# Performance work log

Measured on AMD Instinct MI355X. Metric: run time of the kernel, lower is better.

## Reference

```python
import jax, jax.numpy as jnp
import numpy as np

EPS = 1e-5

def _bilinear_sample(xb, ys, xs):
    # xb: [C,H,W]; ys, xs: [H,W] float sample coordinates (zero outside bounds)
    C, H, W = xb.shape
    y0 = jnp.floor(ys); x0 = jnp.floor(xs)
    y1 = y0 + 1.0;      x1 = x0 + 1.0
    wy1 = ys - y0; wy0 = 1.0 - wy1
    wx1 = xs - x0; wx0 = 1.0 - wx1
    def g(yi, xi):
        valid = (yi >= 0) & (yi < H) & (xi >= 0) & (xi < W)
        yc = jnp.clip(yi, 0, H - 1).astype(jnp.int32)
        xc = jnp.clip(xi, 0, W - 1).astype(jnp.int32)
        return xb[:, yc, xc] * valid[None].astype(xb.dtype)  # [C,H,W]
    return (g(y0, x0) * (wy0 * wx0)[None] + g(y0, x1) * (wy0 * wx1)[None]
          + g(y1, x0) * (wy1 * wx0)[None] + g(y1, x1) * (wy1 * wx1)[None])

def _deform_conv2d(x, offset, mask, w, b):
    # x:[B,C,H,W] offset:[B,18,H,W] mask:[B,9,H,W] w:[Co,C,3,3] b:[Co]
    B, C, H, W = x.shape
    Co = w.shape[0]
    ii = jnp.arange(H, dtype=x.dtype)[:, None]
    jj = jnp.arange(W, dtype=x.dtype)[None, :]
    cols = []
    for k in range(9):  # fixed 3x3 kernel positions, row-major (dy=offset[2k], dx=offset[2k+1])
        ky, kx = k // 3 - 1, k % 3 - 1
        ys = ii + ky + offset[:, 2 * k]      # [B,H,W]
        xs = jj + kx + offset[:, 2 * k + 1]
        v = jax.vmap(_bilinear_sample)(x, ys, xs)  # [B,C,H,W]
        cols.append(v * mask[:, k][:, None])
    cols = jnp.stack(cols, axis=1)               # [B,9,C,H,W]
    out = jnp.einsum('bkchw,ock->bohw', cols, w.reshape(Co, C, 9))
    return out + b[None, :, None, None]

def setup_inputs() -> dict:
    key = jax.random.key(0)
    k1, k2, k3, k4 = jax.random.split(key, 4)
    B, Cin, Cout, H, W = 8, 64, 64, 128, 128
    x = jax.random.normal(k1, (B, Cin, H, W), dtype=jnp.float32)
    # offset/mask conv: small weights so learned offsets stay O(1) pixels;
    # bias[18:]=2.0 as in the module's init (masks start near sigmoid(2))
    w_off = jax.random.normal(k2, (27, Cin, 3, 3), dtype=jnp.float32) * 0.01
    b_off = jnp.concatenate([jnp.zeros((18,), jnp.float32), jnp.full((9,), 2.0, jnp.float32)])
    w_dcn = jax.random.normal(k3, (Cout, Cin, 3, 3), dtype=jnp.float32) / np.sqrt(Cin * 9)
    b_dcn = jax.random.normal(k4, (Cout,), dtype=jnp.float32) * 0.01
    return {"x": x, "w_off": w_off, "b_off": b_off, "w_dcn": w_dcn, "b_dcn": b_dcn}

def reference(x, w_off, b_off, w_dcn, b_dcn):
    dn = ('NCHW', 'OIHW', 'NCHW')
    om = jax.lax.conv_general_dilated(x, w_off, (1, 1), 'SAME', dimension_numbers=dn)
    om = om + b_off[None, :, None, None]
    offset = om[:, :18]
    mask = jax.nn.sigmoid(om[:, 18:])
    y = _deform_conv2d(x, offset, mask, w_dcn, b_dcn)
    # InstanceNorm2d (affine=False, biased variance) + ReLU
    mu = jnp.mean(y, axis=(2, 3), keepdims=True)
    var = jnp.var(y, axis=(2, 3), keepdims=True)
    y = (y - mu) * jax.lax.rsqrt(var + EPS)
    return jax.nn.relu(y)
```

## Files before the change

kernel.cpp:

```cpp
#include <hip/hip_runtime.h>
#include <hip/hip_bf16.h>

#define BB   8
#define CIN  64
#define COUT 64
#define HH   128
#define WW   128
#define HWSZ (HH * WW)

typedef short bf16x8 __attribute__((ext_vector_type(8)));
typedef float f32x4  __attribute__((ext_vector_type(4)));
typedef float f32x2  __attribute__((ext_vector_type(2)));

__device__ __forceinline__ unsigned f2bf_u(float f) {
    unsigned u = __float_as_uint(f);
    return (u + 0x7fffu + ((u >> 16) & 1u)) >> 16;
}

__device__ __forceinline__ unsigned comb2(unsigned a, unsigned b, unsigned c, unsigned d,
                                          f32x2 W0, f32x2 W1, f32x2 W2, f32x2 W3) {
    f32x2 A = {__uint_as_float(a << 16), __uint_as_float(a & 0xffff0000u)};
    f32x2 B = {__uint_as_float(b << 16), __uint_as_float(b & 0xffff0000u)};
    f32x2 C = {__uint_as_float(c << 16), __uint_as_float(c & 0xffff0000u)};
    f32x2 D = {__uint_as_float(d << 16), __uint_as_float(d & 0xffff0000u)};
    f32x2 r = A * W0;
    r += B * W1;
    r += C * W2;
    r += D * W3;
    __hip_bfloat162 h = __float22bfloat162_rn(make_float2(r.x, r.y));
    return *(const unsigned*)&h;
}

__global__ __launch_bounds__(256) void k_tr(const float* __restrict__ x,
                                            const float* __restrict__ wd,
                                            const float* __restrict__ wof,
                                            unsigned short* __restrict__ xT,
                                            unsigned short* __restrict__ wdT,
                                            unsigned short* __restrict__ wofT)
{
    const int t = threadIdx.x;
    const int id = blockIdx.x;
    if (id >= 512) {
        int base = (id - 512) * 256 + t;
#pragma unroll
        for (int j = 0; j < 4; ++j) {
            int idx = base + j * 16384;
            if (idx < 36864) {
                int k = idx >> 12, rem = idx & 4095, co = rem >> 6, c = rem & 63;
                wdT[idx] = (unsigned short)f2bf_u(wd[(co * 64 + c) * 9 + k]);
            } else if (idx < 55296) {
                int jj = idx - 36864;
                int k = jj >> 11, rem = jj & 2047, o = rem >> 6, c = rem & 63;
                wofT[jj] = (o < 27) ? (unsigned short)f2bf_u(wof[(o * 64 + c) * 9 + k]) : 0;
            }
        }
        return;
    }
    __shared__ unsigned short tile[256 * 66];
    const int b = id & 7;
    const int p0 = (id >> 3) * 256;
#pragma unroll
    for (int i = 0; i < 16; ++i) {
        int c = i * 4 + (t >> 6);
        int pl = (t & 63) * 4;
        float4 v = *(const float4*)(x + (((size_t)b * 64 + c) << 14) + p0 + pl);
        tile[(pl + 0) * 66 + c] = (unsigned short)f2bf_u(v.x);
        tile[(pl + 1) * 66 + c] = (unsigned short)f2bf_u(v.y);
        tile[(pl + 2) * 66 + c] = (unsigned short)f2bf_u(v.z);
        tile[(pl + 3) * 66 + c] = (unsigned short)f2bf_u(v.w);
    }
    __syncthreads();
#pragma unroll
    for (int i = 0; i < 8; ++i) {
        int idd = i * 256 + t;
        int pt = idd >> 3, ck = idd & 7;
        const unsigned* srcp = (const unsigned*)&tile[pt * 66 + ck * 8];
        uint4 r;
        r.x = srcp[0]; r.y = srcp[1]; r.z = srcp[2]; r.w = srcp[3];
        *(uint4*)(xT + ((size_t)b << 20) + (size_t)(p0 + pt) * 64 + ck * 8) = r;
    }
}

__global__ __launch_bounds__(256, 2) void k_off(
    const unsigned short* __restrict__ xT, const unsigned short* __restrict__ wofT,
    const float* __restrict__ bof, float* __restrict__ om)
{
    __shared__ unsigned short tile[8 * 521 * 8];
    const int t = threadIdx.x;
    const int lane = t & 63, wv = t >> 6;
    const int q = lane >> 4, l15 = lane & 15;
    const int b = blockIdx.x & 7;
    const int xblk = blockIdx.x >> 3;
    const int h0 = xblk * 2;
    const int r0 = h0 - 1;
    const unsigned short* xb = xT + ((size_t)b << 20);

#pragma unroll
    for (int i = 0; i < 17; ++i) {
        int id = i * 256 + t;
        if (id < 4160) {
            int m = id & 7, lin = id >> 3;
            int row = lin / 130, col = lin % 130;
            int gy = r0 + row, gx = col - 1;
            uint4 v = {0u, 0u, 0u, 0u};
            if (((unsigned)gy < (unsigned)HH) && ((unsigned)gx < (unsigned)WW))
                v = *(const uint4*)(xb + ((size_t)(gy * WW + gx) << 6) + m * 8);
            *(uint4*)&tile[(m * 521 + lin) * 8] = v;
        }
    }
    __syncthreads();

    const int hrow = h0 + (wv >> 1);
    const int c0 = (wv & 1) * 64;

    f32x4 acc[2][4];
#pragma unroll
    for (int mt = 0; mt < 2; ++mt)
#pragma unroll
        for (int nt = 0; nt < 4; ++nt) acc[mt][nt] = (f32x4){0.f, 0.f, 0.f, 0.f};

#pragma unroll
    for (int k = 0; k < 9; ++k) {
        const int ky = k / 3 - 1, kx = k % 3 - 1;
        const int trow = (hrow - h0) + ky + 1;
        const unsigned short* wk = wofT + k * 2048;
#pragma unroll
        for (int ks = 0; ks < 2; ++ks) {
            bf16x8 af[2], bfr[4];
#pragma unroll
            for (int mt = 0; mt < 2; ++mt)
                af[mt] = *(const bf16x8*)(wk + (mt * 16 + l15) * 64 + ks * 32 + q * 8);
#pragma unroll
            for (int nt = 0; nt < 4; ++nt) {
                int tc = c0 + nt * 16 + l15 + kx + 1;
                bfr[nt] = *(const bf16x8*)&tile[((ks * 4 + q) * 521 + trow * 130 + tc) * 8];
            }
#pragma unroll
            for (int mt = 0; mt < 2; ++mt)
#pragma unroll
                for (int nt = 0; nt < 4; ++nt)
                    acc[mt][nt] = __builtin_amdgcn_mfma_f32_16x16x32_bf16(
                        af[mt], bfr[nt], acc[mt][nt], 0, 0, 0);
        }
    }

    const int p0 = xblk * 256 + wv * 64;
    float* omb = om + (size_t)b * 27 * HWSZ;
#pragma unroll
    for (int mt = 0; mt < 2; ++mt)
#pragma unroll
        for (int r = 0; r < 4; ++r) {
            int o = mt * 16 + q * 4 + r;
            if (o < 27) {
                float bias = bof[o];
#pragma unroll
                for (int nt = 0; nt < 4; ++nt) {
                    int pp = p0 + nt * 16 + l15;
                    float v = acc[mt][nt][r] + bias;
                    if (o >= 18) v = 1.f / (1.f + __expf(-v));
                    omb[(size_t)o * HWSZ + pp] = v;
                }
            }
        }
}

__global__ __launch_bounds__(256, 2) void k_dcn(
    const unsigned short* __restrict__ xT, const float* __restrict__ om,
    const unsigned short* __restrict__ wdT, const float* __restrict__ bd,
    float* __restrict__ out, float2* __restrict__ sums)
{
    __shared__ unsigned short col_sh[4][64 * 80];
    __shared__ unsigned       adr_sh[4][4][64];
    __shared__ float4         w_sh[4][64];
    __shared__ float          redS[4][64];
    __shared__ float          redQ[4][64];

    const int t = threadIdx.x;
    const int lane = t & 63, wv = t >> 6;
    const int q = lane >> 4, l15 = lane & 15;
    const int b = blockIdx.x & 7;
    const int pblk = (blockIdx.x >> 3) * 256;
    const int p = pblk + t;
    const int h = p >> 7, w = p & 127;
    const char* xbB = (const char*)(xT + ((size_t)b << 20));
    const float* omp = om + (size_t)b * 27 * HWSZ + p;
    const int gck = lane & 7;

    f32x4 acc[4][4];
#pragma unroll
    for (int mt = 0; mt < 4; ++mt)
#pragma unroll
        for (int nt = 0; nt < 4; ++nt) acc[mt][nt] = (f32x4){0.f, 0.f, 0.f, 0.f};

#define LOADG(P, g) { \
    int pt_ = (g) * 8 + (lane >> 3); \
    unsigned o0_ = adr_sh[wv][0][pt_]; \
    unsigned o1_ = adr_sh[wv][1][pt_]; \
    unsigned o2_ = adr_sh[wv][2][pt_]; \
    unsigned o3_ = adr_sh[wv][3][pt_]; \
    int bo_ = gck * 16; \
    P[0] = *(const uint4*)(xbB + o0_ + bo_); \
    P[1] = *(const uint4*)(xbB + o1_ + bo_); \
    P[2] = *(const uint4*)(xbB + o2_ + bo_); \
    P[3] = *(const uint4*)(xbB + o3_ + bo_); }

#define COMBG(P, g) { \
    int pt_ = (g) * 8 + (lane >> 3); \
    float4 w4_ = w_sh[wv][pt_]; \
    f32x2 W0_ = {w4_.x, w4_.x}, W1_ = {w4_.y, w4_.y}; \
    f32x2 W2_ = {w4_.z, w4_.z}, W3_ = {w4_.w, w4_.w}; \
    uint4 R_; \
    R_.x = comb2(P[0].x, P[1].x, P[2].x, P[3].x, W0_, W1_, W2_, W3_); \
    R_.y = comb2(P[0].y, P[1].y, P[2].y, P[3].y, W0_, W1_, W2_, W3_); \
    R_.z = comb2(P[0].z, P[1].z, P[2].z, P[3].z, W0_, W1_, W2_, W3_); \
    R_.w = comb2(P[0].w, P[1].w, P[2].w, P[3].w, W0_, W1_, W2_, W3_); \
    *(uint4*)&col_sh[wv][pt_ * 80 + gck * 8] = R_; }

    float offy = omp[0];
    float offx = omp[HWSZ];
    float mk   = omp[18 * HWSZ];

    for (int k = 0; k < 9; ++k) {
        float ys = (float)(h + (k / 3) - 1) + offy;
        float xs = (float)(w + (k % 3) - 1) + offx;
        float fy0 = floorf(ys), fx0 = floorf(xs);
        float wy1 = ys - fy0, wx1 = xs - fx0;
        float wy0 = 1.f - wy1, wx0 = 1.f - wx1;
        int y0 = (int)fy0, x0 = (int)fx0;
        int y1 = y0 + 1, x1 = x0 + 1;
        bool vy0 = (y0 >= 0) && (y0 < HH), vy1 = (y1 >= 0) && (y1 < HH);
        bool vx0 = (x0 >= 0) && (x0 < WW), vx1 = (x1 >= 0) && (x1 < WW);
        int y0c = min(max(y0, 0), HH - 1), y1c = min(max(y1, 0), HH - 1);
        int x0c = min(max(x0, 0), WW - 1), x1c = min(max(x1, 0), WW - 1);
        adr_sh[wv][0][lane] = (unsigned)((y0c * WW + x0c) << 7);
        adr_sh[wv][1][lane] = (unsigned)((y0c * WW + x1c) << 7);
        adr_sh[wv][2][lane] = (unsigned)((y1c * WW + x0c) << 7);
        adr_sh[wv][3][lane] = (unsigned)((y1c * WW + x1c) << 7);
        w_sh[wv][lane] = make_float4((vy0 && vx0) ? mk * wy0 * wx0 : 0.f,
                                     (vy0 && vx1) ? mk * wy0 * wx1 : 0.f,
                                     (vy1 && vx0) ? mk * wy1 * wx0 : 0.f,
                                     (vy1 && vx1) ? mk * wy1 * wx1 : 0.f);
        int kn = (k < 8) ? k + 1 : 8;
        offy = omp[(2 * kn) * HWSZ];
        offx = omp[(2 * kn + 1) * HWSZ];
        mk   = omp[(18 + kn) * HWSZ];
        __builtin_amdgcn_wave_barrier();

        const unsigned short* wk = wdT + k * 4096;
        bf16x8 af[2][4];
#pragma unroll
        for (int ks = 0; ks < 2; ++ks)
#pragma unroll
            for (int mt = 0; mt < 4; ++mt)
                af[ks][mt] = *(const bf16x8*)(wk + (mt * 16 + l15) * 64 + ks * 32 + q * 8);

        uint4 pb[3][4];
        LOADG(pb[0], 0);
        LOADG(pb[1], 1);
#pragma unroll
        for (int g = 0; g < 8; ++g) {
            if (g + 2 < 8) LOADG(pb[(g + 2) % 3], g + 2);
            COMBG(pb[g % 3], g);
        }
        __builtin_amdgcn_wave_barrier();

#pragma unroll
        for (int ks = 0; ks < 2; ++ks) {
            bf16x8 bfr[4];
#pragma unroll
            for (int nt = 0; nt < 4; ++nt)
                bfr[nt] = *(const bf16x8*)&col_sh[wv][(nt * 16 + l15) * 80 + ks * 32 + q * 8];
#pragma unroll
            for (int mt = 0; mt < 4; ++mt)
#pragma unroll
                for (int nt = 0; nt < 4; ++nt)
                    acc[mt][nt] = __builtin_amdgcn_mfma_f32_16x16x32_bf16(
                        af[ks][mt], bfr[nt], acc[mt][nt], 0, 0, 0);
        }
    }
#undef LOADG
#undef COMBG

    const int p0 = pblk + wv * 64;
    float* outb = out + (size_t)b * COUT * HWSZ;
#pragma unroll
    for (int mt = 0; mt < 4; ++mt)
#pragma unroll
        for (int r = 0; r < 4; ++r) {
            int co = mt * 16 + q * 4 + r;
            float bias = bd[co];
            float s = 0.f, qq = 0.f;
#pragma unroll
            for (int nt = 0; nt < 4; ++nt) {
                float v = acc[mt][nt][r] + bias;
                outb[(size_t)co * HWSZ + p0 + nt * 16 + l15] = v;
                s += v; qq += v * v;
            }
#pragma unroll
            for (int m = 1; m < 16; m <<= 1) {
                s += __shfl_xor(s, m);
                qq += __shfl_xor(qq, m);
            }
            if (l15 == 0) { redS[wv][co] = s; redQ[wv][co] = qq; }
        }
    __syncthreads();
    if (t < 64) {
        float S = redS[0][t] + redS[1][t] + redS[2][t] + redS[3][t];
        float Q = redQ[0][t] + redQ[1][t] + redQ[2][t] + redQ[3][t];
        atomicAdd(&sums[b * 64 + t].x, S);
        atomicAdd(&sums[b * 64 + t].y, Q);
    }
}

__global__ __launch_bounds__(256) void k_norm(float* __restrict__ out,
                                              const float2* __restrict__ sums)
{
    const int id = blockIdx.x;
    const int b = id & 7;
    const int rest = id >> 3;
    const int co = rest >> 4;
    const int off = rest & 15;
    const int bco = b * 64 + co;
    const int i = (bco << 12) + off * 256 + threadIdx.x;
    float2 sq = sums[bco];
    float mu  = sq.x * (1.f / (float)HWSZ);
    float var = sq.y * (1.f / (float)HWSZ) - mu * mu;
    float rstd = rsqrtf(var + 1e-5f);
    float4* o4 = (float4*)out;
    float4 v = o4[i];
    v.x = fmaxf((v.x - mu) * rstd, 0.f);
    v.y = fmaxf((v.y - mu) * rstd, 0.f);
    v.z = fmaxf((v.z - mu) * rstd, 0.f);
    v.w = fmaxf((v.w - mu) * rstd, 0.f);
    o4[i] = v;
}

extern "C" void kernel_launch(void* const* d_in, const int* in_sizes, int n_in,
                              void* d_out, int out_size, void* d_ws, size_t ws_size,
                              hipStream_t stream) {
    const float* x   = (const float*)d_in[0];
    const float* wof = (const float*)d_in[1];
    const float* bof = (const float*)d_in[2];
    const float* wd  = (const float*)d_in[3];
    const float* bd  = (const float*)d_in[4];
    float* out = (float*)d_out;

    char* ws = (char*)d_ws;
    unsigned short* xT   = (unsigned short*)ws;
    float*          om   = (float*)(ws + 16777216);
    unsigned short* wdT  = (unsigned short*)(ws + 30932992);
    unsigned short* wofT = (unsigned short*)(ws + 31006720);
    float2*         sums = (float2*)(ws + 31043584);

    hipMemsetAsync(sums, 0, 4096, stream);
    k_tr    <<<576, 256, 0, stream>>>(x, wd, wof, xT, wdT, wofT);
    k_off   <<<512, 256, 0, stream>>>(xT, wofT, bof, om);
    k_dcn   <<<512, 256, 0, stream>>>(xT, om, wdT, bd, out, sums);
    k_norm  <<<8192, 256, 0, stream>>>(out, (const float2*)sums);
}
```

Before: 173.6 us.

## Shuffle sample addresses via registers, shrink LDS, raise DCN occupancy, fold memset

Per-pixel bilinear addresses and weights are now passed between lanes with __shfl instead of being staged through per-wave LDS arrays. The column tile padding shrinks from 80 to 72 elements and launch bounds go from 2 to 4 blocks per CU. Together these cut LDS use and aim for more resident waves to hide gather latency. The sums buffer is now zeroed inside k_tr instead of by a separate hipMemsetAsync, removing one stream operation. Risks are register pressure at the higher occupancy target and more shuffle instructions in the inner loop.

```diff
diff --git a/kernel.cpp b/kernel.cpp
--- a/kernel.cpp
+++ b/kernel.cpp
@@ -36,11 +36,13 @@
                                             const float* __restrict__ wof,
                                             unsigned short* __restrict__ xT,
                                             unsigned short* __restrict__ wdT,
-                                            unsigned short* __restrict__ wofT)
+                                            unsigned short* __restrict__ wofT,
+                                            float4* __restrict__ sums4)
 {
     const int t = threadIdx.x;
     const int id = blockIdx.x;
     if (id >= 512) {
+        if (id == 512) sums4[t] = make_float4(0.f, 0.f, 0.f, 0.f);
         int base = (id - 512) * 256 + t;
 #pragma unroll
         for (int j = 0; j < 4; ++j) {
@@ -164,14 +166,12 @@
         }
 }
 
-__global__ __launch_bounds__(256, 2) void k_dcn(
+__global__ __launch_bounds__(256, 4) void k_dcn(
     const unsigned short* __restrict__ xT, const float* __restrict__ om,
     const unsigned short* __restrict__ wdT, const float* __restrict__ bd,
     float* __restrict__ out, float2* __restrict__ sums)
 {
-    __shared__ unsigned short col_sh[4][64 * 80];
-    __shared__ unsigned       adr_sh[4][4][64];
-    __shared__ float4         w_sh[4][64];
+    __shared__ unsigned short col_sh[4][64 * 72];
     __shared__ float          redS[4][64];
     __shared__ float          redQ[4][64];
 
@@ -194,10 +194,10 @@
 
 #define LOADG(P, g) { \
     int pt_ = (g) * 8 + (lane >> 3); \
-    unsigned o0_ = adr_sh[wv][0][pt_]; \
-    unsigned o1_ = adr_sh[wv][1][pt_]; \
-    unsigned o2_ = adr_sh[wv][2][pt_]; \
-    unsigned o3_ = adr_sh[wv][3][pt_]; \
+    unsigned o0_ = (unsigned)__shfl((int)a0, pt_); \
+    unsigned o1_ = (unsigned)__shfl((int)a1, pt_); \
+    unsigned o2_ = (unsigned)__shfl((int)a2, pt_); \
+    unsigned o3_ = (unsigned)__shfl((int)a3, pt_); \
     int bo_ = gck * 16; \
     P[0] = *(const uint4*)(xbB + o0_ + bo_); \
     P[1] = *(const uint4*)(xbB + o1_ + bo_); \
@@ -206,15 +206,16 @@
 
 #define COMBG(P, g) { \
     int pt_ = (g) * 8 + (lane >> 3); \
-    float4 w4_ = w_sh[wv][pt_]; \
-    f32x2 W0_ = {w4_.x, w4_.x}, W1_ = {w4_.y, w4_.y}; \
-    f32x2 W2_ = {w4_.z, w4_.z}, W3_ = {w4_.w, w4_.w}; \
+    float w0_ = __shfl(wb0, pt_), w1_ = __shfl(wb1, pt_); \
+    float w2_ = __shfl(wb2, pt_), w3_ = __shfl(wb3, pt_); \
+    f32x2 W0_ = {w0_, w0_}, W1_ = {w1_, w1_}; \
+    f32x2 W2_ = {w2_, w2_}, W3_ = {w3_, w3_}; \
     uint4 R_; \
     R_.x = comb2(P[0].x, P[1].x, P[2].x, P[3].x, W0_, W1_, W2_, W3_); \
     R_.y = comb2(P[0].y, P[1].y, P[2].y, P[3].y, W0_, W1_, W2_, W3_); \
     R_.z = comb2(P[0].z, P[1].z, P[2].z, P[3].z, W0_, W1_, W2_, W3_); \
     R_.w = comb2(P[0].w, P[1].w, P[2].w, P[3].w, W0_, W1_, W2_, W3_); \
-    *(uint4*)&col_sh[wv][pt_ * 80 + gck * 8] = R_; }
+    *(uint4*)&col_sh[wv][pt_ * 72 + gck * 8] = R_; }
 
     float offy = omp[0];
     float offx = omp[HWSZ];
@@ -232,19 +233,18 @@
         bool vx0 = (x0 >= 0) && (x0 < WW), vx1 = (x1 >= 0) && (x1 < WW);
         int y0c = min(max(y0, 0), HH - 1), y1c = min(max(y1, 0), HH - 1);
         int x0c = min(max(x0, 0), WW - 1), x1c = min(max(x1, 0), WW - 1);
-        adr_sh[wv][0][lane] = (unsigned)((y0c * WW + x0c) << 7);
-        adr_sh[wv][1][lane] = (unsigned)((y0c * WW + x1c) << 7);
-        adr_sh[wv][2][lane] = (unsigned)((y1c * WW + x0c) << 7);
-        adr_sh[wv][3][lane] = (unsigned)((y1c * WW + x1c) << 7);
-        w_sh[wv][lane] = make_float4((vy0 && vx0) ? mk * wy0 * wx0 : 0.f,
-                                     (vy0 && vx1) ? mk * wy0 * wx1 : 0.f,
-                                     (vy1 && vx0) ? mk * wy1 * wx0 : 0.f,
-                                     (vy1 && vx1) ? mk * wy1 * wx1 : 0.f);
+        unsigned a0 = (unsigned)((y0c * WW + x0c) << 7);
+        unsigned a1 = (unsigned)((y0c * WW + x1c) << 7);
+        unsigned a2 = (unsigned)((y1c * WW + x0c) << 7);
+        unsigned a3 = (unsigned)((y1c * WW + x1c) << 7);
+        float wb0 = (vy0 && vx0) ? mk * wy0 * wx0 : 0.f;
+        float wb1 = (vy0 && vx1) ? mk * wy0 * wx1 : 0.f;
+        float wb2 = (vy1 && vx0) ? mk * wy1 * wx0 : 0.f;
+        float wb3 = (vy1 && vx1) ? mk * wy1 * wx1 : 0.f;
         int kn = (k < 8) ? k + 1 : 8;
         offy = omp[(2 * kn) * HWSZ];
         offx = omp[(2 * kn + 1) * HWSZ];
         mk   = omp[(18 + kn) * HWSZ];
-        __builtin_amdgcn_wave_barrier();
 
         const unsigned short* wk = wdT + k * 4096;
         bf16x8 af[2][4];
@@ -269,7 +269,7 @@
             bf16x8 bfr[4];
 #pragma unroll
             for (int nt = 0; nt < 4; ++nt)
-                bfr[nt] = *(const bf16x8*)&col_sh[wv][(nt * 16 + l15) * 80 + ks * 32 + q * 8];
+                bfr[nt] = *(const bf16x8*)&col_sh[wv][(nt * 16 + l15) * 72 + ks * 32 + q * 8];
 #pragma unroll
             for (int mt = 0; mt < 4; ++mt)
 #pragma unroll
@@ -277,6 +277,7 @@
                     acc[mt][nt] = __builtin_amdgcn_mfma_f32_16x16x32_bf16(
                         af[ks][mt], bfr[nt], acc[mt][nt], 0, 0, 0);
         }
+        __builtin_amdgcn_wave_barrier();
     }
 #undef LOADG
 #undef COMBG
@@ -352,8 +353,7 @@
     unsigned short* wofT = (unsigned short*)(ws + 31006720);
     float2*         sums = (float2*)(ws + 31043584);
 
-    hipMemsetAsync(sums, 0, 4096, stream);
-    k_tr    <<<576, 256, 0, stream>>>(x, wd, wof, xT, wdT, wofT);
+    k_tr    <<<576, 256, 0, stream>>>(x, wd, wof, xT, wdT, wofT, (float4*)sums);
     k_off   <<<512, 256, 0, stream>>>(xT, wofT, bof, om);
     k_dcn   <<<512, 256, 0, stream>>>(xT, om, wdT, bd, out, sums);
     k_norm  <<<8192, 256, 0, stream>>>(out, (const float2*)sums);
```

Measured after the change: 239.8 us. 38.1% more time.

## Switch intermediate storage and bilinear combine from bf16 to fp16 packed math

Applied to the files above, without the earlier changes.

Stores the transposed input and weights as fp16 instead of bf16, runs the MFMAs as f16, and does the four-tap bilinear combine in packed half2 arithmetic instead of unpacking to fp32 and repacking. This removes the unpack and round-trip conversion ALU work in the gather-combine hot loop. The sums memset is folded into the transpose kernel to drop one launch. fp16 has a narrower range than bf16, and the interpolation is now accumulated in half precision, which may reduce accuracy.

```diff
diff --git a/kernel.cpp b/kernel.cpp
--- a/kernel.cpp
+++ b/kernel.cpp
@@ -1,5 +1,5 @@
 #include <hip/hip_runtime.h>
-#include <hip/hip_bf16.h>
+#include <hip/hip_fp16.h>
 
 #define BB   8
 #define CIN  64
@@ -8,27 +8,27 @@
 #define WW   128
 #define HWSZ (HH * WW)
 
-typedef short bf16x8 __attribute__((ext_vector_type(8)));
-typedef float f32x4  __attribute__((ext_vector_type(4)));
-typedef float f32x2  __attribute__((ext_vector_type(2)));
-
-__device__ __forceinline__ unsigned f2bf_u(float f) {
-    unsigned u = __float_as_uint(f);
-    return (u + 0x7fffu + ((u >> 16) & 1u)) >> 16;
-}
-
-__device__ __forceinline__ unsigned comb2(unsigned a, unsigned b, unsigned c, unsigned d,
-                                          f32x2 W0, f32x2 W1, f32x2 W2, f32x2 W3) {
-    f32x2 A = {__uint_as_float(a << 16), __uint_as_float(a & 0xffff0000u)};
-    f32x2 B = {__uint_as_float(b << 16), __uint_as_float(b & 0xffff0000u)};
-    f32x2 C = {__uint_as_float(c << 16), __uint_as_float(c & 0xffff0000u)};
-    f32x2 D = {__uint_as_float(d << 16), __uint_as_float(d & 0xffff0000u)};
-    f32x2 r = A * W0;
+typedef _Float16 f16x8 __attribute__((ext_vector_type(8)));
+typedef _Float16 h2v   __attribute__((ext_vector_type(2)));
+typedef float    f32x4 __attribute__((ext_vector_type(4)));
+
+__device__ __forceinline__ unsigned short f2h_u(float f) {
+    __half h = __float2half(f);
+    return __half_as_ushort(h);
+}
+__device__ __forceinline__ unsigned duph(float f) {
+    unsigned u = (unsigned)f2h_u(f);
+    return u | (u << 16);
+}
+
+__device__ __forceinline__ unsigned comb2h(unsigned a, unsigned b, unsigned c, unsigned d,
+                                           h2v W0, h2v W1, h2v W2, h2v W3) {
+    h2v A = *(h2v*)&a, B = *(h2v*)&b, C = *(h2v*)&c, D = *(h2v*)&d;
+    h2v r = A * W0;
     r += B * W1;
     r += C * W2;
     r += D * W3;
-    __hip_bfloat162 h = __float22bfloat162_rn(make_float2(r.x, r.y));
-    return *(const unsigned*)&h;
+    return *(unsigned*)&r;
 }
 
 __global__ __launch_bounds__(256) void k_tr(const float* __restrict__ x,
@@ -36,22 +36,24 @@
                                             const float* __restrict__ wof,
                                             unsigned short* __restrict__ xT,
                                             unsigned short* __restrict__ wdT,
-                                            unsigned short* __restrict__ wofT)
+                                            unsigned short* __restrict__ wofT,
+                                            float4* __restrict__ sums4)
 {
     const int t = threadIdx.x;
     const int id = blockIdx.x;
     if (id >= 512) {
+        if (id == 512) sums4[t] = make_float4(0.f, 0.f, 0.f, 0.f);
         int base = (id - 512) * 256 + t;
 #pragma unroll
         for (int j = 0; j < 4; ++j) {
             int idx = base + j * 16384;
             if (idx < 36864) {
                 int k = idx >> 12, rem = idx & 4095, co = rem >> 6, c = rem & 63;
-                wdT[idx] = (unsigned short)f2bf_u(wd[(co * 64 + c) * 9 + k]);
+                wdT[idx] = f2h_u(wd[(co * 64 + c) * 9 + k]);
             } else if (idx < 55296) {
                 int jj = idx - 36864;
                 int k = jj >> 11, rem = jj & 2047, o = rem >> 6, c = rem & 63;
-                wofT[jj] = (o < 27) ? (unsigned short)f2bf_u(wof[(o * 64 + c) * 9 + k]) : 0;
+                wofT[jj] = (o < 27) ? f2h_u(wof[(o * 64 + c) * 9 + k]) : 0;
             }
         }
         return;
@@ -64,10 +66,10 @@
         int c = i * 4 + (t >> 6);
         int pl = (t & 63) * 4;
         float4 v = *(const float4*)(x + (((size_t)b * 64 + c) << 14) + p0 + pl);
-        tile[(pl + 0) * 66 + c] = (unsigned short)f2bf_u(v.x);
-        tile[(pl + 1) * 66 + c] = (unsigned short)f2bf_u(v.y);
-        tile[(pl + 2) * 66 + c] = (unsigned short)f2bf_u(v.z);
-        tile[(pl + 3) * 66 + c] = (unsigned short)f2bf_u(v.w);
+        tile[(pl + 0) * 66 + c] = f2h_u(v.x);
+        tile[(pl + 1) * 66 + c] = f2h_u(v.y);
+        tile[(pl + 2) * 66 + c] = f2h_u(v.z);
+        tile[(pl + 3) * 66 + c] = f2h_u(v.w);
     }
     __syncthreads();
 #pragma unroll
@@ -126,20 +128,20 @@
         const unsigned short* wk = wofT + k * 2048;
 #pragma unroll
         for (int ks = 0; ks < 2; ++ks) {
-            bf16x8 af[2], bfr[4];
+            f16x8 af[2], bfr[4];
 #pragma unroll
             for (int mt = 0; mt < 2; ++mt)
-                af[mt] = *(const bf16x8*)(wk + (mt * 16 + l15) * 64 + ks * 32 + q * 8);
+                af[mt] = *(const f16x8*)(wk + (mt * 16 + l15) * 64 + ks * 32 + q * 8);
 #pragma unroll
             for (int nt = 0; nt < 4; ++nt) {
                 int tc = c0 + nt * 16 + l15 + kx + 1;
-                bfr[nt] = *(const bf16x8*)&tile[((ks * 4 + q) * 521 + trow * 130 + tc) * 8];
+                bfr[nt] = *(const f16x8*)&tile[((ks * 4 + q) * 521 + trow * 130 + tc) * 8];
             }
 #pragma unroll
             for (int mt = 0; mt < 2; ++mt)
 #pragma unroll
                 for (int nt = 0; nt < 4; ++nt)
-                    acc[mt][nt] = __builtin_amdgcn_mfma_f32_16x16x32_bf16(
+                    acc[mt][nt] = __builtin_amdgcn_mfma_f32_16x16x32_f16(
                         af[mt], bfr[nt], acc[mt][nt], 0, 0, 0);
         }
     }
@@ -171,7 +173,7 @@
 {
     __shared__ unsigned short col_sh[4][64 * 80];
     __shared__ unsigned       adr_sh[4][4][64];
-    __shared__ float4         w_sh[4][64];
+    __shared__ uint4          w_sh[4][64];
     __shared__ float          redS[4][64];
     __shared__ float          redQ[4][64];
 
@@ -206,14 +208,14 @@
 
 #define COMBG(P, g) { \
     int pt_ = (g) * 8 + (lane >> 3); \
-    float4 w4_ = w_sh[wv][pt_]; \
-    f32x2 W0_ = {w4_.x, w4_.x}, W1_ = {w4_.y, w4_.y}; \
-    f32x2 W2_ = {w4_.z, w4_.z}, W3_ = {w4_.w, w4_.w}; \
+    uint4 pw_ = w_sh[wv][pt_]; \
+    h2v W0_ = *(h2v*)&pw_.x, W1_ = *(h2v*)&pw_.y; \
+    h2v W2_ = *(h2v*)&pw_.z, W3_ = *(h2v*)&pw_.w; \
     uint4 R_; \
-    R_.x = comb2(P[0].x, P[1].x, P[2].x, P[3].x, W0_, W1_, W2_, W3_); \
-    R_.y = comb2(P[0].y, P[1].y, P[2].y, P[3].y, W0_, W1_, W2_, W3_); \
-    R_.z = comb2(P[0].z, P[1].z, P[2].z, P[3].z, W0_, W1_, W2_, W3_); \
-    R_.w = comb2(P[0].w, P[1].w, P[2].w, P[3].w, W0_, W1_, W2_, W3_); \
+    R_.x = comb2h(P[0].x, P[1].x, P[2].x, P[3].x, W0_, W1_, W2_, W3_); \
+    R_.y = comb2h(P[0].y, P[1].y, P[2].y, P[3].y, W0_, W1_, W2_, W3_); \
+    R_.z = comb2h(P[0].z, P[1].z, P[2].z, P[3].z, W0_, W1_, W2_, W3_); \
+    R_.w = comb2h(P[0].w, P[1].w, P[2].w, P[3].w, W0_, W1_, W2_, W3_); \
     *(uint4*)&col_sh[wv][pt_ * 80 + gck * 8] = R_; }
 
     float offy = omp[0];
@@ -236,10 +238,11 @@
         adr_sh[wv][1][lane] = (unsigned)((y0c * WW + x1c) << 7);
         adr_sh[wv][2][lane] = (unsigned)((y1c * WW + x0c) << 7);
         adr_sh[wv][3][lane] = (unsigned)((y1c * WW + x1c) << 7);
-        w_sh[wv][lane] = make_float4((vy0 && vx0) ? mk * wy0 * wx0 : 0.f,
-                                     (vy0 && vx1) ? mk * wy0 * wx1 : 0.f,
-                                     (vy1 && vx0) ? mk * wy1 * wx0 : 0.f,
-                                     (vy1 && vx1) ? mk * wy1 * wx1 : 0.f);
+        w_sh[wv][lane] = make_uint4(
+            duph((vy0 && vx0) ? mk * wy0 * wx0 : 0.f),
+            duph((vy0 && vx1) ? mk * wy0 * wx1 : 0.f),
+            duph((vy1 && vx0) ? mk * wy1 * wx0 : 0.f),
+            duph((vy1 && vx1) ? mk * wy1 * wx1 : 0.f));
         int kn = (k < 8) ? k + 1 : 8;
         offy = omp[(2 * kn) * HWSZ];
         offx = omp[(2 * kn + 1) * HWSZ];
@@ -247,12 +250,12 @@
         __builtin_amdgcn_wave_barrier();
 
         const unsigned short* wk = wdT + k * 4096;
-        bf16x8 af[2][4];
+        f16x8 af[2][4];
 #pragma unroll
         for (int ks = 0; ks < 2; ++ks)
 #pragma unroll
             for (int mt = 0; mt < 4; ++mt)
-                af[ks][mt] = *(const bf16x8*)(wk + (mt * 16 + l15) * 64 + ks * 32 + q * 8);
+                af[ks][mt] = *(const f16x8*)(wk + (mt * 16 + l15) * 64 + ks * 32 + q * 8);
 
         uint4 pb[3][4];
         LOADG(pb[0], 0);
@@ -266,15 +269,15 @@
 
 #pragma unroll
         for (int ks = 0; ks < 2; ++ks) {
-            bf16x8 bfr[4];
+            f16x8 bfr[4];
 #pragma unroll
             for (int nt = 0; nt < 4; ++nt)
-                bfr[nt] = *(const bf16x8*)&col_sh[wv][(nt * 16 + l15) * 80 + ks * 32 + q * 8];
+                bfr[nt] = *(const f16x8*)&col_sh[wv][(nt * 16 + l15) * 80 + ks * 32 + q * 8];
 #pragma unroll
             for (int mt = 0; mt < 4; ++mt)
 #pragma unroll
                 for (int nt = 0; nt < 4; ++nt)
-                    acc[mt][nt] = __builtin_amdgcn_mfma_f32_16x16x32_bf16(
+                    acc[mt][nt] = __builtin_amdgcn_mfma_f32_16x16x32_f16(
                         af[ks][mt], bfr[nt], acc[mt][nt], 0, 0, 0);
         }
     }
@@ -352,8 +355,7 @@
     unsigned short* wofT = (unsigned short*)(ws + 31006720);
     float2*         sums = (float2*)(ws + 31043584);
 
-    hipMemsetAsync(sums, 0, 4096, stream);
-    k_tr    <<<576, 256, 0, stream>>>(x, wd, wof, xT, wdT, wofT);
+    k_tr    <<<576, 256, 0, stream>>>(x, wd, wof, xT, wdT, wofT, (float4*)sums);
     k_off   <<<512, 256, 0, stream>>>(xT, wofT, bof, om);
     k_dcn   <<<512, 256, 0, stream>>>(xT, om, wdT, bd, out, sums);
     k_norm  <<<8192, 256, 0, stream>>>(out, (const float2*)sums);
```

Measured after the change: 171.3 us. About the same (-1.3%).
